# Performance work log

Measured on AMD Instinct MI355X. Metric: run time of the kernel, lower is better.

The kernel has to match this reference:

```python
import jax, jax.numpy as jnp
import numpy as np
from jax import lax

B, T, C, F_IN = 32, 2048, 64, 8
CONV_F, ATT_D, HID, N_CLS = 32, 32, 128, 4


def layer_norm(x, scale, bias, eps=1e-6):
    mu = jnp.mean(x, axis=-1, keepdims=True)
    var = jnp.mean(jnp.square(x - mu), axis=-1, keepdims=True)
    return (x - mu) * lax.rsqrt(var + eps) * scale + bias


def setup_inputs() -> dict:
    key = jax.random.key(0)
    ks = jax.random.split(key, 12)
    s = lambda *sh: 1.0 / np.sqrt(sh[-2] if len(sh) > 1 else sh[-1])
    inp = {
        "X": jax.random.normal(ks[0], (B, T, C, F_IN), jnp.float32),
        "conv_w": jax.random.normal(ks[1], (5, 1, F_IN, CONV_F), jnp.float32) * 0.1,
        "conv_b": jnp.zeros((CONV_F,), jnp.float32),
        "ln1_s": jnp.ones((CONV_F,), jnp.float32),
        "ln1_b": jnp.zeros((CONV_F,), jnp.float32),
        "q_w": jax.random.normal(ks[2], (CONV_F, ATT_D), jnp.float32) * s(CONV_F, ATT_D),
        "q_b": jnp.zeros((ATT_D,), jnp.float32),
        "k_w": jax.random.normal(ks[3], (CONV_F, ATT_D), jnp.float32) * s(CONV_F, ATT_D),
        "k_b": jnp.zeros((ATT_D,), jnp.float32),
        "ca_w": jax.random.normal(ks[4], (C, C), jnp.float32) * s(C, C),
        "ca_b": jnp.zeros((C,), jnp.float32),
        "mix_w": jax.random.normal(ks[5], (C * CONV_F, HID), jnp.float32) * s(C * CONV_F, HID),
        "mix_b": jnp.zeros((HID,), jnp.float32),
        "ln2_s": jnp.ones((HID,), jnp.float32),
        "ln2_b": jnp.zeros((HID,), jnp.float32),
        "decay_logit": jnp.full((1, HID), 2.0, jnp.float32),
        "fc_w": jax.random.normal(ks[6], (HID, HID), jnp.float32) * s(HID, HID),
        "fc_b": jnp.zeros((HID,), jnp.float32),
        "out_w": jax.random.normal(ks[7], (HID, N_CLS), jnp.float32) * s(HID, N_CLS),
        "out_b": jnp.zeros((N_CLS,), jnp.float32),
        "train": False,
    }
    return inp


def reference(X, conv_w, conv_b, ln1_s, ln1_b, q_w, q_b, k_w, k_b, ca_w, ca_b,
              mix_w, mix_b, ln2_s, ln2_b, decay_logit, fc_w, fc_b, out_w, out_b, train):
    # eval mode (train=False): no input noise, dropout is identity
    # conv: (B,T,C,F_in) -> (B,T/2,C,32), SAME padding, stride (2,1)
    Xc = lax.conv_general_dilated(X, conv_w, window_strides=(2, 1), padding='SAME',
                                  dimension_numbers=('NHWC', 'HWIO', 'NHWC')) + conv_b
    Xc = jax.nn.relu(Xc)
    Xc = layer_norm(Xc, ln1_s, ln1_b)

    # dynamic graph attention over channel axis
    x_spat = jnp.mean(Xc, axis=1)                         # (B,C,32)
    q = x_spat @ q_w + q_b
    k = x_spat @ k_w + k_b
    adj = jax.nn.softmax(jnp.einsum('bcf,bdf->bcd', q, k) / jnp.sqrt(jnp.float32(ATT_D)), axis=-1)
    Xg = jnp.einsum('bcd,btdf->btcf', adj, Xc)            # (B,T2,C,32)

    # channel gating
    ca = jax.nn.sigmoid(jnp.mean(Xc, axis=(1, 3)) @ ca_w + ca_b)  # (B,C)
    Xr = Xg * ca[:, None, :, None] + Xc

    b, t2 = Xr.shape[0], Xr.shape[1]
    Xf = Xr.reshape(b, t2, -1)                            # (B,T2,2048)
    Xm = jax.nn.relu(Xf @ mix_w + mix_b)
    Xm = layer_norm(Xm, ln2_s, ln2_b)                     # (B,T2,128)

    # LIF spiking recurrence over time
    decay = jax.nn.sigmoid(decay_logit)                   # (1,128)

    def step(mem, xt):
        mem = mem * decay + xt
        spk = (mem - 0.5 > 0).astype(mem.dtype)
        mem = mem - spk * 0.5
        return mem, spk

    _, spk_seq = lax.scan(step, jnp.zeros((b, HID), Xm.dtype), jnp.swapaxes(Xm, 0, 1))
    spk_seq = jnp.swapaxes(spk_seq, 0, 1)                 # (B,T2,128)

    feat = jnp.mean(spk_seq, axis=1)                      # (B,128)
    feat = jax.nn.relu(feat @ fc_w + fc_b)
    logits = feat @ out_w + out_b
    return logits, jnp.mean(spk_seq)
```

## Files before the change

kernel.cpp:

```cpp
#include <hip/hip_runtime.h>
#include <math.h>

#define B_    32
#define T_    2048
#define T2_   1024
#define C_    64
#define FI_   8
#define FO_   32
#define K_    2048
#define H_    128

typedef unsigned short u16;
typedef short bf16x8 __attribute__((ext_vector_type(8)));
typedef float f32x4 __attribute__((ext_vector_type(4)));

#define OFF_XSP  ((size_t)0)
#define OFF_WTH  ((size_t)67108864)
#define OFF_A    ((size_t)77594624)
#define OFF_XM   ((size_t)77725696)

__device__ __forceinline__ float bft(float x) {
  unsigned u = __float_as_uint(x);
  u = (u + 0x7fffu + ((u >> 16) & 1u)) & 0xffff0000u;
  return __uint_as_float(u);
}
__device__ __forceinline__ unsigned bfpack(float a, float b) {
  unsigned ua = __float_as_uint(a); ua = (ua + 0x7fffu + ((ua >> 16) & 1u)) >> 16;
  unsigned ub = __float_as_uint(b); ub = (ub + 0x7fffu + ((ub >> 16) & 1u)) & 0xffff0000u;
  return ua | ub;
}
__device__ __forceinline__ unsigned cvtpk(float a, float b) {
  unsigned r;
  asm("v_cvt_pk_bf16_f32 %0, %1, %2" : "=v"(r) : "v"(a), "v"(b));
  return r;
}
__device__ __forceinline__ bf16x8 packhi(const float4& x0, const float4& x1) {
  uint4 hv = make_uint4(cvtpk(x0.x, x0.y), cvtpk(x0.z, x0.w),
                        cvtpk(x1.x, x1.y), cvtpk(x1.z, x1.w));
  return *(bf16x8*)&hv;
}
__device__ __forceinline__ void pack8(const float4& x0, const float4& x1,
                                      bf16x8& h, bf16x8& l) {
  float v[8] = {x0.x, x0.y, x0.z, x0.w, x1.x, x1.y, x1.z, x1.w};
  unsigned hu[4], lu[4];
#pragma unroll
  for (int p = 0; p < 4; ++p) {
    const float a = v[2*p], b2 = v[2*p+1];
    const unsigned ph = cvtpk(a, b2);
    hu[p] = ph;
    const float fa_ = __uint_as_float(ph << 16);
    const float fb_ = __uint_as_float(ph & 0xffff0000u);
    lu[p] = cvtpk(a - fa_, b2 - fb_);
  }
  uint4 hv = make_uint4(hu[0], hu[1], hu[2], hu[3]);
  uint4 lv = make_uint4(lu[0], lu[1], lu[2], lu[3]);
  h = *(bf16x8*)&hv; l = *(bf16x8*)&lv;
}

__device__ __forceinline__ void glds16(const u16* g, u16* l) {
  auto gp = reinterpret_cast<const __attribute__((address_space(1))) unsigned int*>(
      reinterpret_cast<uintptr_t>(g));
  auto lp = reinterpret_cast<__attribute__((address_space(3))) unsigned int*>(
      reinterpret_cast<uintptr_t>(l));
  __builtin_amdgcn_global_load_lds(gp, lp, 16, 0, 0);
}

__global__ __launch_bounds__(256, 3) void k1_conv_ln(
    const float* __restrict__ X, const float* __restrict__ Wc,
    const float* __restrict__ bc, const float* __restrict__ g1,
    const float* __restrict__ be1, float* __restrict__ xsp)
{
  __shared__ float xred[4][1056];
  const int tid = threadIdx.x;
  const int w = tid >> 6, lane = tid & 63;
  const int q = lane >> 4, cl = lane & 15;
  const int chalf = w & 1, rng = w >> 1;
  const int b = blockIdx.y, tile = blockIdx.x;
  const int cbase = chalf * 32;

  bf16x8 Wh[2][2], Wl[2][2];
#pragma unroll
  for (int s = 0; s < 2; ++s)
#pragma unroll
    for (int mt = 0; mt < 2; ++mt) {
      const int f = mt * 16 + cl;
      float x8[8];
#pragma unroll
      for (int j = 0; j < 8; ++j) {
        float wv;
        if (s == 0) {
          wv = Wc[(q * 8 + j) * 32 + f];
        } else {
          wv = 0.f;
          if (q == 0) wv = Wc[(32 + j) * 32 + f];
          if (q == 1 && j == 0) wv = bc[f];
        }
        x8[j] = wv;
      }
      unsigned hu[4], lu[4];
#pragma unroll
      for (int p = 0; p < 4; ++p) {
        const float a0 = x8[2*p], a1 = x8[2*p+1];
        hu[p] = bfpack(a0, a1);
        lu[p] = bfpack(a0 - bft(a0), a1 - bft(a1));
      }
      uint4 hv = make_uint4(hu[0], hu[1], hu[2], hu[3]);
      uint4 lv = make_uint4(lu[0], lu[1], lu[2], lu[3]);
      Wh[s][mt] = *(bf16x8*)&hv;
      Wl[s][mt] = *(bf16x8*)&lv;
    }

  float g1r[2][4], be1r[2][4];
#pragma unroll
  for (int mt = 0; mt < 2; ++mt)
#pragma unroll
    for (int r = 0; r < 4; ++r) {
      const int f = mt * 16 + 4 * q + r;
      g1r[mt][r] = g1[f];
      be1r[mt][r] = be1[f];
    }

  float sacc[2][2][4];
#pragma unroll
  for (int mt = 0; mt < 2; ++mt)
#pragma unroll
    for (int nt = 0; nt < 2; ++nt)
#pragma unroll
      for (int r = 0; r < 4; ++r) sacc[mt][nt][r] = 0.f;

  const float* Xb = X + (size_t)b * T_ * C_ * FI_;
  const float4 z4f = make_float4(0.f, 0.f, 0.f, 0.f);
  const int c0g = cbase + cl, c1g = cbase + 16 + cl;

  float4 A0, A1, A2, A3, A4, A5, A6, A7;
  float4 B0, B1, B2, B3, B4, B5, B6, B7;

  auto LD = [&](int it, float4& v0, float4& v1, float4& v2, float4& v3,
                        float4& v4, float4& v5, float4& v6, float4& v7) {
    const int t2 = tile * 16 + rng * 8 + it;
    const int r0 = 2 * t2 + q - 1, r1 = 2 * t2 + 3;
    const bool ok0 = (r0 >= 0) && (r0 < T_);
    const bool ok1 = (q == 0) && (r1 < T_);
    v0 = z4f; v1 = z4f; v2 = z4f; v3 = z4f;
    v4 = z4f; v5 = z4f; v6 = z4f; v7 = z4f;
    if (ok0) {
      const float* p = Xb + (size_t)r0 * (C_ * FI_);
      v0 = *(const float4*)(p + c0g * FI_);
      v1 = *(const float4*)(p + c0g * FI_ + 4);
      v4 = *(const float4*)(p + c1g * FI_);
      v5 = *(const float4*)(p + c1g * FI_ + 4);
    }
    if (ok1) {
      const float* p = Xb + (size_t)r1 * (C_ * FI_);
      v2 = *(const float4*)(p + c0g * FI_);
      v3 = *(const float4*)(p + c0g * FI_ + 4);
      v6 = *(const float4*)(p + c1g * FI_);
      v7 = *(const float4*)(p + c1g * FI_ + 4);
    }
  };

  auto CMP = [&](const float4& v0, const float4& v1, const float4& v2,
                 const float4& v3, const float4& v4, const float4& v5,
                 const float4& v6, const float4& v7) {
    f32x4 acc[2][2];
#pragma unroll
    for (int mt = 0; mt < 2; ++mt)
#pragma unroll
      for (int nt = 0; nt < 2; ++nt) acc[mt][nt] = (f32x4){0.f,0.f,0.f,0.f};

#pragma unroll
    for (int nt = 0; nt < 2; ++nt) {
      bf16x8 Bh0 = packhi(nt ? v4 : v0, nt ? v5 : v1);
      bf16x8 Bh1 = packhi(nt ? v6 : v2, nt ? v7 : v3);
      if (q == 1) Bh1[0] = (short)0x3F80;
#pragma unroll
      for (int mt = 0; mt < 2; ++mt) {
        acc[mt][nt] = __builtin_amdgcn_mfma_f32_16x16x32_bf16(Wh[0][mt], Bh0, acc[mt][nt], 0, 0, 0);
        acc[mt][nt] = __builtin_amdgcn_mfma_f32_16x16x32_bf16(Wl[0][mt], Bh0, acc[mt][nt], 0, 0, 0);
        acc[mt][nt] = __builtin_amdgcn_mfma_f32_16x16x32_bf16(Wh[1][mt], Bh1, acc[mt][nt], 0, 0, 0);
        acc[mt][nt] = __builtin_amdgcn_mfma_f32_16x16x32_bf16(Wl[1][mt], Bh1, acc[mt][nt], 0, 0, 0);
      }
    }
#pragma unroll
    for (int nt = 0; nt < 2; ++nt) {
      float v[2][4];
      float s1 = 0.f, s2 = 0.f;
#pragma unroll
      for (int mt = 0; mt < 2; ++mt)
#pragma unroll
        for (int r = 0; r < 4; ++r) {
          const float vv = fmaxf(acc[mt][nt][r], 0.f);
          v[mt][r] = vv; s1 += vv; s2 = fmaf(vv, vv, s2);
        }
      s1 += __shfl_xor(s1, 16); s2 += __shfl_xor(s2, 16);
      s1 += __shfl_xor(s1, 32); s2 += __shfl_xor(s2, 32);
      const float mu = s1 * (1.f / 32.f);
      const float var = s2 * (1.f / 32.f) - mu * mu;
      const float rs = rsqrtf(var + 1e-6f);
#pragma unroll
      for (int mt = 0; mt < 2; ++mt)
#pragma unroll
        for (int r = 0; r < 4; ++r)
          sacc[mt][nt][r] += (v[mt][r] - mu) * rs * g1r[mt][r] + be1r[mt][r];
    }
  };

  LD(0, A0, A1, A2, A3, A4, A5, A6, A7);
#pragma unroll 1
  for (int it = 0; it < 8; it += 2) {
    if (it + 1 < 8) LD(it + 1, B0, B1, B2, B3, B4, B5, B6, B7);
    CMP(A0, A1, A2, A3, A4, A5, A6, A7);
    if (it + 2 < 8) LD(it + 2, A0, A1, A2, A3, A4, A5, A6, A7);
    CMP(B0, B1, B2, B3, B4, B5, B6, B7);
  }

#pragma unroll
  for (int mt = 0; mt < 2; ++mt)
#pragma unroll
    for (int nt = 0; nt < 2; ++nt)
#pragma unroll
      for (int r = 0; r < 4; ++r)
        xred[w][(nt * 16 + cl) * 33 + mt * 16 + 4 * q + r] = sacc[mt][nt][r];
  __syncthreads();
  if (w < 2) {
#pragma unroll
    for (int mt = 0; mt < 2; ++mt)
#pragma unroll
      for (int nt = 0; nt < 2; ++nt)
#pragma unroll
        for (int r = 0; r < 4; ++r) {
          const int idx = (nt * 16 + cl) * 33 + mt * 16 + 4 * q + r;
          const float vv = xred[w][idx] + xred[w + 2][idx];
          xsp[((size_t)b * 64 + tile) * 2048 +
              (size_t)(w * 32 + nt * 16 + cl) * 32 + mt * 16 + 4 * q + r] = vv;
        }
  }
}

__global__ __launch_bounds__(256) void k2_graph(
    const float* __restrict__ xsp, const float* __restrict__ qw,
    const float* __restrict__ qb, const float* __restrict__ kw,
    const float* __restrict__ kb, const float* __restrict__ caw,
    const float* __restrict__ cab, float* __restrict__ Aout)
{
  __shared__ float xs[64 * 32];
  __shared__ float qs[64][32];
  __shared__ float ks[64][32];
  __shared__ float sc[64][64];
  __shared__ float cain[64];
  __shared__ float cav[64];
  const int tid = threadIdx.x;
  const int b = blockIdx.x;

  for (int idx = tid; idx < 2048; idx += 256) {
    float s = 0.f;
    for (int p = 0; p < 64; ++p) s += xsp[((size_t)b * 64 + p) * 2048 + idx];
    xs[idx] = s * (1.f / (float)T2_);
  }
  __syncthreads();

  if (tid < 64) {
    float s = 0.f;
#pragma unroll
    for (int f = 0; f < 32; ++f) s += xs[tid * 32 + f];
    cain[tid] = s * (1.f / 32.f);
  }
  {
    const int cc = tid >> 2, part = tid & 3;
    float aq[8], ak[8];
#pragma unroll
    for (int j = 0; j < 8; ++j) { aq[j] = qb[part*8+j]; ak[j] = kb[part*8+j]; }
    for (int f = 0; f < 32; ++f) {
      const float xv = xs[cc * 32 + f];
#pragma unroll
      for (int j = 0; j < 8; ++j) {
        aq[j] = fmaf(xv, qw[f * 32 + part*8+j], aq[j]);
        ak[j] = fmaf(xv, kw[f * 32 + part*8+j], ak[j]);
      }
    }
#pragma unroll
    for (int j = 0; j < 8; ++j) { qs[cc][part*8+j] = aq[j]; ks[cc][part*8+j] = ak[j]; }
  }
  __syncthreads();
  {
    const int cc = tid >> 2, part = tid & 3;
    for (int dd = part * 16; dd < part * 16 + 16; ++dd) {
      float s = 0.f;
#pragma unroll
      for (int e = 0; e < 32; ++e) s = fmaf(qs[cc][e], ks[dd][e], s);
      sc[cc][dd] = s * 0.1767766953f;
    }
  }
  __syncthreads();
  if (tid < 64) {
    const int cc = tid;
    float m = -1e30f;
    for (int d = 0; d < 64; ++d) m = fmaxf(m, sc[cc][d]);
    float sum = 0.f;
    for (int d = 0; d < 64; ++d) { float e = expf(sc[cc][d] - m); sc[cc][d] = e; sum += e; }
    const float inv = 1.f / sum;
    for (int d = 0; d < 64; ++d) sc[cc][d] *= inv;
    float a = cab[cc];
    for (int d = 0; d < 64; ++d) a = fmaf(cain[d], caw[d * 64 + cc], a);
    cav[cc] = 1.f / (1.f + expf(-a));
  }
  __syncthreads();
  for (int idx = tid; idx < 4096; idx += 256) {
    const int cc = idx >> 6, dd = idx & 63;
    Aout[(size_t)b * 4096 + idx] = cav[cc] * sc[cc][dd] + (cc == dd ? 1.f : 0.f);
  }
}

__global__ __launch_bounds__(256) void k3_weff(
    const float* __restrict__ Aout, const float* __restrict__ mixw,
    u16* __restrict__ Wth)
{
  __shared__ float Ap[4096];
  __shared__ float Ms[2048];
  const int tid = threadIdx.x;
  const int b = blockIdx.x >> 5, ht = blockIdx.x & 31;
  const int d = tid & 63, hl = tid >> 6;
  const int h0 = ht * 4;
  const float* Ab = Aout + (size_t)b * 4096;
#pragma unroll
  for (int l = 0; l < 16; ++l) Ap[tid + 256 * l] = Ab[tid + 256 * l];

  float acc[32];
#pragma unroll
  for (int j = 0; j < 32; ++j) acc[j] = 0.f;

  for (int c0 = 0; c0 < 64; c0 += 16) {
    __syncthreads();
    {
      const int i0 = tid * 8;
#pragma unroll
      for (int qd = 0; qd < 2; ++qd) {
        const int i = i0 + qd * 4;
        const int cc = i >> 7, f = (i >> 2) & 31;
        const float4 v = *(const float4*)&mixw[((size_t)((c0+cc)*32 + f))*128 + h0];
        float* mp = &Ms[cc * 128 + f];
        mp[0] = v.x; mp[32] = v.y; mp[64] = v.z; mp[96] = v.w;
      }
    }
    __syncthreads();
#pragma unroll 4
    for (int cc = 0; cc < 16; ++cc) {
      const float a = Ap[(c0 + cc) * 64 + d];
      const float* mrow = &Ms[cc * 128 + hl * 32];
#pragma unroll
      for (int fq = 0; fq < 8; ++fq) {
        const f32x4 m = *(const f32x4*)&mrow[fq * 4];
        acc[fq*4+0] = fmaf(a, m[0], acc[fq*4+0]);
        acc[fq*4+1] = fmaf(a, m[1], acc[fq*4+1]);
        acc[fq*4+2] = fmaf(a, m[2], acc[fq*4+2]);
        acc[fq*4+3] = fmaf(a, m[3], acc[fq*4+3]);
      }
    }
  }

  const int h = h0 + hl;
  const size_t obase = ((size_t)(b * 64 + d) * 128 + h) * 32;
#pragma unroll
  for (int g = 0; g < 4; ++g) {
    unsigned hq[4];
#pragma unroll
    for (int jj = 0; jj < 4; ++jj)
      hq[jj] = bfpack(acc[8*g + 2*jj], acc[8*g + 2*jj + 1]);
    const int pg = (g ^ hl ^ (ht & 3)) * 8;
    *(uint4*)(Wth + obase + pg) = make_uint4(hq[0], hq[1], hq[2], hq[3]);
  }
}

__global__ __launch_bounds__(256, 2) void k4_fused(
    const float* __restrict__ X, const float* __restrict__ Wc,
    const float* __restrict__ bc, const float* __restrict__ g1,
    const float* __restrict__ be1,
    const u16* __restrict__ Bgh,
    const float* __restrict__ mixb, const float* __restrict__ g2,
    const float* __restrict__ be2, float* __restrict__ Xm)
{
  __shared__ __align__(16) u16 lds[18432];
  __shared__ float part[64 * 8];
  __shared__ float murs[128];

  const int tid = threadIdx.x;
  const int w = tid >> 6, lane = tid & 63;
  const int q = lane >> 4, cl = lane & 15;
  const int x = blockIdx.x;
  const int swz = (x & 7) * 64 + (x >> 3);
  const int b = swz >> 4, mt = swz & 15;
  const int m0 = mt * 64;

  bf16x8 Wh[2][2], Wl[2][2];
#pragma unroll
  for (int s = 0; s < 2; ++s)
#pragma unroll
    for (int m2 = 0; m2 < 2; ++m2) {
      const int f = m2 * 16 + cl;
      float x8[8];
#pragma unroll
      for (int j = 0; j < 8; ++j) {
        float wv;
        if (s == 0) {
          wv = Wc[(q * 8 + j) * 32 + f];
        } else {
          wv = 0.f;
          if (q == 0) wv = Wc[(32 + j) * 32 + f];
          if (q == 1 && j == 0) wv = bc[f];
        }
        x8[j] = wv;
      }
      unsigned hu[4], lu[4];
#pragma unroll
      for (int p = 0; p < 4; ++p) {
        const float a0 = x8[2*p], a1 = x8[2*p+1];
        hu[p] = bfpack(a0, a1);
        lu[p] = bfpack(a0 - bft(a0), a1 - bft(a1));
      }
      uint4 hv = make_uint4(hu[0], hu[1], hu[2], hu[3]);
      uint4 lv = make_uint4(lu[0], lu[1], lu[2], lu[3]);
      Wh[s][m2] = *(bf16x8*)&hv;
      Wl[s][m2] = *(bf16x8*)&lv;
    }
  float g1r[2][4], be1r[2][4];
#pragma unroll
  for (int m2 = 0; m2 < 2; ++m2)
#pragma unroll
    for (int r = 0; r < 4; ++r) {
      const int f = m2 * 16 + 4 * q + r;
      g1r[m2][r] = g1[f];
      be1r[m2][r] = be1[f];
    }

  f32x4 acc[4][2];
#pragma unroll
  for (int i = 0; i < 4; ++i)
#pragma unroll
    for (int j = 0; j < 2; ++j) acc[i][j] = (f32x4){0.f, 0.f, 0.f, 0.f};

  const int lrow = lane >> 2, lg = lane & 3;
  const size_t brow0 = (size_t)b * 262144 + (size_t)(w * 16 + lrow) * 32 + lg * 8;
  const int dA = w * 512;
  const int faA = cl * 40 + q * 8;
  const int faB = cl * 32 + ((q ^ (cl & 3) ^ (cl >> 2)) * 8);
  const float* Xb = X + (size_t)b * T_ * (C_ * FI_);
  const int t2 = m0 + w * 16 + cl;
  const int t2loc = w * 16 + cl;

  const int r0 = 2 * t2 + q - 1, r1 = 2 * t2 + 3;
  const bool ok0 = (r0 >= 0) && (r0 < T_);
  const bool ok1 = (q == 0) && (r1 < T_);
  const float* rp0 = Xb + (size_t)(ok0 ? r0 : 0) * (C_ * FI_);
  const float* rp1 = Xb + (size_t)(ok1 ? r1 : 0) * (C_ * FI_);
  const float4 z4f = make_float4(0.f, 0.f, 0.f, 0.f);

  float4 A0a, A1a, B0a, B1a;
  float4 A0b, A1b, B0b, B1b;

  auto LOADX = [&](float4& X0, float4& X1, float4& Y0, float4& Y1, int c) {
    X0 = z4f; X1 = z4f; Y0 = z4f; Y1 = z4f;
    if (ok0) { const float* p = rp0 + c * FI_; X0 = *(const float4*)p; X1 = *(const float4*)(p + 4); }
    if (ok1) { const float* p = rp1 + c * FI_; Y0 = *(const float4*)p; Y1 = *(const float4*)(p + 4); }
  };

  auto CONV = [&](const float4& X0, const float4& X1,
                  const float4& Y0, const float4& Y1, int nb) {
    bf16x8 Bh0, Bl0, Bh1, Bl1;
    pack8(X0, X1, Bh0, Bl0);
    pack8(Y0, Y1, Bh1, Bl1);
    if (q == 1) Bh1[0] = (short)0x3F80;
    f32x4 ca0 = (f32x4){0.f,0.f,0.f,0.f}, ca1 = ca0;
    ca0 = __builtin_amdgcn_mfma_f32_16x16x32_bf16(Wh[0][0], Bh0, ca0, 0, 0, 0);
    ca1 = __builtin_amdgcn_mfma_f32_16x16x32_bf16(Wh[0][1], Bh0, ca1, 0, 0, 0);
    ca0 = __builtin_amdgcn_mfma_f32_16x16x32_bf16(Wh[0][0], Bl0, ca0, 0, 0, 0);
    ca1 = __builtin_amdgcn_mfma_f32_16x16x32_bf16(Wh[0][1], Bl0, ca1, 0, 0, 0);
    ca0 = __builtin_amdgcn_mfma_f32_16x16x32_bf16(Wl[0][0], Bh0, ca0, 0, 0, 0);
    ca1 = __builtin_amdgcn_mfma_f32_16x16x32_bf16(Wl[0][1], Bh0, ca1, 0, 0, 0);
    ca0 = __builtin_amdgcn_mfma_f32_16x16x32_bf16(Wh[1][0], Bh1, ca0, 0, 0, 0);
    ca1 = __builtin_amdgcn_mfma_f32_16x16x32_bf16(Wh[1][1], Bh1, ca1, 0, 0, 0);
    ca0 = __builtin_amdgcn_mfma_f32_16x16x32_bf16(Wh[1][0], Bl1, ca0, 0, 0, 0);
    ca1 = __builtin_amdgcn_mfma_f32_16x16x32_bf16(Wh[1][1], Bl1, ca1, 0, 0, 0);
    ca0 = __builtin_amdgcn_mfma_f32_16x16x32_bf16(Wl[1][0], Bh1, ca0, 0, 0, 0);
    ca1 = __builtin_amdgcn_mfma_f32_16x16x32_bf16(Wl[1][1], Bh1, ca1, 0, 0, 0);
    float v[2][4];
    float s1 = 0.f, s2 = 0.f;
#pragma unroll
    for (int r = 0; r < 4; ++r) {
      float vv = fmaxf(ca0[r], 0.f); v[0][r] = vv; s1 += vv; s2 = fmaf(vv, vv, s2);
      vv = fmaxf(ca1[r], 0.f);       v[1][r] = vv; s1 += vv; s2 = fmaf(vv, vv, s2);
    }
    s1 += __shfl_xor(s1, 16); s2 += __shfl_xor(s2, 16);
    s1 += __shfl_xor(s1, 32); s2 += __shfl_xor(s2, 32);
    const float mu = s1 * (1.f / 32.f);
    const float var = s2 * (1.f / 32.f) - mu * mu;
    const float rs = rsqrtf(var + 1e-6f);
    const int ab = nb * 5120;
#pragma unroll
    for (int m2 = 0; m2 < 2; ++m2) {
      float y[4];
#pragma unroll
      for (int r = 0; r < 4; ++r)
        y[r] = (v[m2][r] - mu) * rs * g1r[m2][r] + be1r[m2][r];
      const unsigned h0 = cvtpk(y[0], y[1]);
      const unsigned h1 = cvtpk(y[2], y[3]);
      const float f00 = __uint_as_float(h0 << 16);
      const float f01 = __uint_as_float(h0 & 0xffff0000u);
      const float f10 = __uint_as_float(h1 << 16);
      const float f11 = __uint_as_float(h1 & 0xffff0000u);
      const unsigned l0 = cvtpk(y[0] - f00, y[1] - f01);
      const unsigned l1 = cvtpk(y[2] - f10, y[3] - f11);
      const int phys = 2 * m2 + (q >> 1);
      const int off = ab + t2loc * 40 + phys * 8 + (q & 1) * 4;
      *(uint2*)&lds[off] = make_uint2(h0, h1);
      *(uint2*)&lds[off + 2560] = make_uint2(l0, l1);
    }
  };

#define STAGE_B(kt, nb) do {                                                 \
    const int bb_ = 10240 + (nb) * 4096;                                     \
    glds16(Bgh + brow0 + (size_t)(kt) * 4096,        &lds[bb_ + dA]);        \
    glds16(Bgh + brow0 + (size_t)(kt) * 4096 + 2048, &lds[bb_ + 2048 + dA]); \
  } while (0)

  auto GEMM = [&](int nb) {
    const int ab = nb * 5120, bb = 10240 + nb * 4096;
    bf16x8 ah[4], al[4], bh[2];
#pragma unroll
    for (int mf = 0; mf < 4; ++mf) {
      ah[mf] = *(const bf16x8*)&lds[ab + mf * 640 + faA];
      al[mf] = *(const bf16x8*)&lds[ab + 2560 + mf * 640 + faA];
    }
#pragma unroll
    for (int nf = 0; nf < 2; ++nf)
      bh[nf] = *(const bf16x8*)&lds[bb + w * 1024 + nf * 512 + faB];
#pragma unroll
    for (int mf = 0; mf < 4; ++mf)
#pragma unroll
      for (int nf = 0; nf < 2; ++nf) {
        acc[mf][nf] = __builtin_amdgcn_mfma_f32_16x16x32_bf16(ah[mf], bh[nf], acc[mf][nf], 0, 0, 0);
        acc[mf][nf] = __builtin_amdgcn_mfma_f32_16x16x32_bf16(al[mf], bh[nf], acc[mf][nf], 0, 0, 0);
      }
  };

  LOADX(A0a, A1a, B0a, B1a, 0);
  STAGE_B(0, 0);
  LOADX(A0b, A1b, B0b, B1b, 1);
  CONV(A0a, A1a, B0a, B1a, 0);
  __syncthreads();

  for (int kt = 0; kt < 64; kt += 2) {
    if (kt + 2 < 64) LOADX(A0a, A1a, B0a, B1a, kt + 2);
    STAGE_B(kt + 1, 1);
    GEMM(0);
    CONV(A0b, A1b, B0b, B1b, 1);
    __syncthreads();
    if (kt + 3 < 64) LOADX(A0b, A1b, B0b, B1b, kt + 3);
    if (kt + 2 < 64) STAGE_B(kt + 2, 0);
    GEMM(1);
    if (kt + 2 < 64) CONV(A0a, A1a, B0a, B1a, 0);
    __syncthreads();
  }
#undef STAGE_B

  const int c0 = w * 32 + (lane & 15);
  const float bias0 = mixb[c0], bias1 = mixb[c0 + 16];
#pragma unroll
  for (int mf = 0; mf < 4; ++mf)
#pragma unroll
    for (int r = 0; r < 4; ++r) {
      float v0 = fmaxf(acc[mf][0][r] + bias0, 0.f);
      float v1 = fmaxf(acc[mf][1][r] + bias1, 0.f);
      acc[mf][0][r] = v0; acc[mf][1][r] = v1;
      float s1 = v0 + v1, s2 = v0 * v0 + v1 * v1;
      s1 += __shfl_xor(s1, 1);  s2 += __shfl_xor(s2, 1);
      s1 += __shfl_xor(s1, 2);  s2 += __shfl_xor(s2, 2);
      s1 += __shfl_xor(s1, 4);  s2 += __shfl_xor(s2, 4);
      s1 += __shfl_xor(s1, 8);  s2 += __shfl_xor(s2, 8);
      if ((lane & 15) == 0) {
        const int row = mf * 16 + (lane >> 4) * 4 + r;
        part[row * 8 + w * 2] = s1;
        part[row * 8 + w * 2 + 1] = s2;
      }
    }
  __syncthreads();
  if (tid < 64) {
    const float s1 = part[tid*8] + part[tid*8+2] + part[tid*8+4] + part[tid*8+6];
    const float s2 = part[tid*8+1] + part[tid*8+3] + part[tid*8+5] + part[tid*8+7];
    const float mu = s1 * (1.f / 128.f);
    const float var = s2 * (1.f / 128.f) - mu * mu;
    murs[tid * 2] = mu;
    murs[tid * 2 + 1] = rsqrtf(var + 1e-6f);
  }
  __syncthreads();
  const float g20 = g2[c0], g21 = g2[c0 + 16];
  const float b20 = be2[c0], b21 = be2[c0 + 16];
#pragma unroll
  for (int mf = 0; mf < 4; ++mf)
#pragma unroll
    for (int r = 0; r < 4; ++r) {
      const int row = mf * 16 + (lane >> 4) * 4 + r;
      const float mu = murs[row * 2], rs = murs[row * 2 + 1];
      float* op = Xm + (size_t)(b * 1024 + m0 + row) * 128;
      op[c0]      = (acc[mf][0][r] - mu) * rs * g20 + b20;
      op[c0 + 16] = (acc[mf][1][r] - mu) * rs * g21 + b21;
    }
}

__global__ __launch_bounds__(64) void k5_lif(
    const float* __restrict__ Xm, const float* __restrict__ dl,
    float* __restrict__ fs)
{
  const int id = blockIdx.x * 64 + threadIdx.x;
  const int b = id >> 7, h = id & 127;
  const float decay = 1.f / (1.f + expf(-dl[h]));
  float mem = 0.f, cnt = 0.f;
  const float* p = Xm + (size_t)b * T2_ * H_ + h;
#pragma unroll 16
  for (int t = 0; t < T2_; ++t) {
    const float xv = p[(size_t)t * H_];
    mem = fmaf(mem, decay, xv);
    const float sp = ((mem - 0.5f) > 0.f) ? 1.f : 0.f;
    cnt += sp;
    mem -= 0.5f * sp;
  }
  fs[b * H_ + h] = cnt;
}

__global__ __launch_bounds__(256) void k6_head(
    const float* __restrict__ fs, const float* __restrict__ fcw,
    const float* __restrict__ fcb, const float* __restrict__ ow,
    const float* __restrict__ ob, float* __restrict__ out)
{
  __shared__ float f[32 * 128];
  __shared__ float fr[32 * 128];
  __shared__ float red[256];
  const int tid = threadIdx.x;
  float tot = 0.f;
  for (int idx = tid; idx < 4096; idx += 256) {
    const float v = fs[idx];
    f[idx] = v * (1.f / (float)T2_);
    tot += v;
  }
  red[tid] = tot;
  __syncthreads();
  for (int s = 128; s > 0; s >>= 1) {
    if (tid < s) red[tid] += red[tid + s];
    __syncthreads();
  }
  {
    const int bb = tid >> 3, og = tid & 7;
    float a[16];
#pragma unroll
    for (int j = 0; j < 16; ++j) a[j] = fcb[og * 16 + j];
    for (int hh = 0; hh < 128; ++hh) {
      const float fv = f[bb * 128 + hh];
#pragma unroll
      for (int j = 0; j < 16; ++j)
        a[j] = fmaf(fv, fcw[hh * 128 + og * 16 + j], a[j]);
    }
#pragma unroll
    for (int j = 0; j < 16; ++j) fr[bb * 128 + og * 16 + j] = fmaxf(a[j], 0.f);
  }
  __syncthreads();
  if (tid < 128) {
    const int bb = tid >> 2, cls = tid & 3;
    float a = ob[cls];
    for (int o = 0; o < 128; ++o) a = fmaf(fr[bb * 128 + o], ow[o * 4 + cls], a);
    out[bb * 4 + cls] = a;
  }
  if (tid == 0) out[128] = red[0] * (1.f / (4096.f * 1024.f));
}

extern "C" void kernel_launch(void* const* d_in, const int* in_sizes, int n_in,
                              void* d_out, int out_size, void* d_ws, size_t ws_size,
                              hipStream_t stream) {
  const float* X     = (const float*)d_in[0];
  const float* convw = (const float*)d_in[1];
  const float* convb = (const float*)d_in[2];
  const float* ln1s  = (const float*)d_in[3];
  const float* ln1b  = (const float*)d_in[4];
  const float* qw    = (const float*)d_in[5];
  const float* qb    = (const float*)d_in[6];
  const float* kw    = (const float*)d_in[7];
  const float* kb    = (const float*)d_in[8];
  const float* caw   = (const float*)d_in[9];
  const float* cab   = (const float*)d_in[10];
  const float* mixw  = (const float*)d_in[11];
  const float* mixb  = (const float*)d_in[12];
  const float* ln2s  = (const float*)d_in[13];
  const float* ln2b  = (const float*)d_in[14];
  const float* dl    = (const float*)d_in[15];
  const float* fcw   = (const float*)d_in[16];
  const float* fcb   = (const float*)d_in[17];
  const float* outw  = (const float*)d_in[18];
  const float* outb  = (const float*)d_in[19];

  float* ws  = (float*)d_ws;
  float* xsp = ws + OFF_XSP;
  u16* Wth   = (u16*)(ws + OFF_WTH);
  float* Aou = ws + OFF_A;
  float* Xm  = ws + OFF_XM;
  float* fs  = ws + OFF_A;

  dim3 g1(64, 32);
  k1_conv_ln<<<g1, 256, 0, stream>>>(X, convw, convb, ln1s, ln1b, xsp);
  k2_graph<<<32, 256, 0, stream>>>(xsp, qw, qb, kw, kb, caw, cab, Aou);
  k3_weff<<<1024, 256, 0, stream>>>(Aou, mixw, Wth);
  k4_fused<<<512, 256, 0, stream>>>(X, convw, convb, ln1s, ln1b,
                                    Wth, mixb, ln2s, ln2b, Xm);
  k5_lif<<<64, 64, 0, stream>>>(Xm, dl, fs);
  k6_head<<<1, 256, 0, stream>>>(fs, fcw, fcb, outw, outb, (float*)d_out);
}
```

Baseline: 292.9 us.

## Split k4 K-loop across two wave groups with LDS reduction

Doubles the k4_fused block to 512 threads. Two groups of four waves each take half of the 64 K-steps, using separate LDS buffers. The partial accumulators are then summed through LDS before the bias, ReLU, LayerNorm and store epilogue. The aim is more waves per tile to hide latency in the conv+GEMM pipeline. The cost is a doubled LDS footprint, an extra exchange and barrier, and half the threads idle in the epilogue.

```diff
diff --git a/kernel.cpp b/kernel.cpp
--- a/kernel.cpp
+++ b/kernel.cpp
@@ -371,7 +371,7 @@
   }
 }
 
-__global__ __launch_bounds__(256, 2) void k4_fused(
+__global__ __launch_bounds__(512) void k4_fused(
     const float* __restrict__ X, const float* __restrict__ Wc,
     const float* __restrict__ bc, const float* __restrict__ g1,
     const float* __restrict__ be1,
@@ -379,17 +379,20 @@
     const float* __restrict__ mixb, const float* __restrict__ g2,
     const float* __restrict__ be2, float* __restrict__ Xm)
 {
-  __shared__ __align__(16) u16 lds[18432];
+  __shared__ __align__(16) u16 lds[36864];
   __shared__ float part[64 * 8];
   __shared__ float murs[128];
 
   const int tid = threadIdx.x;
   const int w = tid >> 6, lane = tid & 63;
+  const int wv = w & 3, g = w >> 2;
   const int q = lane >> 4, cl = lane & 15;
   const int x = blockIdx.x;
   const int swz = (x & 7) * 64 + (x >> 3);
   const int b = swz >> 4, mt = swz & 15;
   const int m0 = mt * 64;
+  const int ks0 = g * 32;
+  const int GB = g * 18432;
 
   bf16x8 Wh[2][2], Wl[2][2];
 #pragma unroll
@@ -400,15 +403,15 @@
       float x8[8];
 #pragma unroll
       for (int j = 0; j < 8; ++j) {
-        float wv;
+        float wvx;
         if (s == 0) {
-          wv = Wc[(q * 8 + j) * 32 + f];
+          wvx = Wc[(q * 8 + j) * 32 + f];
         } else {
-          wv = 0.f;
-          if (q == 0) wv = Wc[(32 + j) * 32 + f];
-          if (q == 1 && j == 0) wv = bc[f];
+          wvx = 0.f;
+          if (q == 0) wvx = Wc[(32 + j) * 32 + f];
+          if (q == 1 && j == 0) wvx = bc[f];
         }
-        x8[j] = wv;
+        x8[j] = wvx;
       }
       unsigned hu[4], lu[4];
 #pragma unroll
@@ -439,13 +442,13 @@
     for (int j = 0; j < 2; ++j) acc[i][j] = (f32x4){0.f, 0.f, 0.f, 0.f};
 
   const int lrow = lane >> 2, lg = lane & 3;
-  const size_t brow0 = (size_t)b * 262144 + (size_t)(w * 16 + lrow) * 32 + lg * 8;
-  const int dA = w * 512;
+  const size_t brow0 = (size_t)b * 262144 + (size_t)(wv * 16 + lrow) * 32 + lg * 8;
+  const int dA = wv * 512;
   const int faA = cl * 40 + q * 8;
   const int faB = cl * 32 + ((q ^ (cl & 3) ^ (cl >> 2)) * 8);
   const float* Xb = X + (size_t)b * T_ * (C_ * FI_);
-  const int t2 = m0 + w * 16 + cl;
-  const int t2loc = w * 16 + cl;
+  const int t2 = m0 + wv * 16 + cl;
+  const int t2loc = wv * 16 + cl;
 
   const int r0 = 2 * t2 + q - 1, r1 = 2 * t2 + 3;
   const bool ok0 = (r0 >= 0) && (r0 < T_);
@@ -494,7 +497,7 @@
     const float mu = s1 * (1.f / 32.f);
     const float var = s2 * (1.f / 32.f) - mu * mu;
     const float rs = rsqrtf(var + 1e-6f);
-    const int ab = nb * 5120;
+    const int ab = GB + nb * 5120;
 #pragma unroll
     for (int m2 = 0; m2 < 2; ++m2) {
       float y[4];
@@ -516,14 +519,14 @@
     }
   };
 
-#define STAGE_B(kt, nb) do {                                                 \
-    const int bb_ = 10240 + (nb) * 4096;                                     \
-    glds16(Bgh + brow0 + (size_t)(kt) * 4096,        &lds[bb_ + dA]);        \
-    glds16(Bgh + brow0 + (size_t)(kt) * 4096 + 2048, &lds[bb_ + 2048 + dA]); \
+#define STAGE_B(ktg, nb) do {                                                \
+    const int bb_ = GB + 10240 + (nb) * 4096;                                \
+    glds16(Bgh + brow0 + (size_t)(ktg) * 4096,        &lds[bb_ + dA]);       \
+    glds16(Bgh + brow0 + (size_t)(ktg) * 4096 + 2048, &lds[bb_ + 2048 + dA]);\
   } while (0)
 
   auto GEMM = [&](int nb) {
-    const int ab = nb * 5120, bb = 10240 + nb * 4096;
+    const int ab = GB + nb * 5120, bb = GB + 10240 + nb * 4096;
     bf16x8 ah[4], al[4], bh[2];
 #pragma unroll
     for (int mf = 0; mf < 4; ++mf) {
@@ -532,7 +535,7 @@
     }
 #pragma unroll
     for (int nf = 0; nf < 2; ++nf)
-      bh[nf] = *(const bf16x8*)&lds[bb + w * 1024 + nf * 512 + faB];
+      bh[nf] = *(const bf16x8*)&lds[bb + wv * 1024 + nf * 512 + faB];
 #pragma unroll
     for (int mf = 0; mf < 4; ++mf)
 #pragma unroll
@@ -542,46 +545,70 @@
       }
   };
 
-  LOADX(A0a, A1a, B0a, B1a, 0);
-  STAGE_B(0, 0);
-  LOADX(A0b, A1b, B0b, B1b, 1);
+  LOADX(A0a, A1a, B0a, B1a, ks0 + 0);
+  STAGE_B(ks0 + 0, 0);
+  LOADX(A0b, A1b, B0b, B1b, ks0 + 1);
   CONV(A0a, A1a, B0a, B1a, 0);
   __syncthreads();
 
-  for (int kt = 0; kt < 64; kt += 2) {
-    if (kt + 2 < 64) LOADX(A0a, A1a, B0a, B1a, kt + 2);
-    STAGE_B(kt + 1, 1);
+  for (int kt = 0; kt < 32; kt += 2) {
+    if (kt + 2 < 32) LOADX(A0a, A1a, B0a, B1a, ks0 + kt + 2);
+    STAGE_B(ks0 + kt + 1, 1);
     GEMM(0);
     CONV(A0b, A1b, B0b, B1b, 1);
     __syncthreads();
-    if (kt + 3 < 64) LOADX(A0b, A1b, B0b, B1b, kt + 3);
-    if (kt + 2 < 64) STAGE_B(kt + 2, 0);
+    if (kt + 3 < 32) LOADX(A0b, A1b, B0b, B1b, ks0 + kt + 3);
+    if (kt + 2 < 32) STAGE_B(ks0 + kt + 2, 0);
     GEMM(1);
-    if (kt + 2 < 64) CONV(A0a, A1a, B0a, B1a, 0);
+    if (kt + 2 < 32) CONV(A0a, A1a, B0a, B1a, 0);
     __syncthreads();
   }
 #undef STAGE_B
 
-  const int c0 = w * 32 + (lane & 15);
+  float* exch = (float*)lds;
+  if (g == 1) {
+    const int l8 = tid & 255;
+#pragma unroll
+    for (int mf = 0; mf < 4; ++mf)
+#pragma unroll
+      for (int nf = 0; nf < 2; ++nf)
+#pragma unroll
+        for (int r = 0; r < 4; ++r)
+          exch[l8 * 33 + mf * 8 + nf * 4 + r] = acc[mf][nf][r];
+  }
+  __syncthreads();
+  if (g == 0) {
+#pragma unroll
+    for (int mf = 0; mf < 4; ++mf)
+#pragma unroll
+      for (int nf = 0; nf < 2; ++nf)
+#pragma unroll
+        for (int r = 0; r < 4; ++r)
+          acc[mf][nf][r] += exch[tid * 33 + mf * 8 + nf * 4 + r];
+  }
+
+  const int c0 = wv * 32 + (lane & 15);
   const float bias0 = mixb[c0], bias1 = mixb[c0 + 16];
-#pragma unroll
-  for (int mf = 0; mf < 4; ++mf)
-#pragma unroll
-    for (int r = 0; r < 4; ++r) {
-      float v0 = fmaxf(acc[mf][0][r] + bias0, 0.f);
-      float v1 = fmaxf(acc[mf][1][r] + bias1, 0.f);
-      acc[mf][0][r] = v0; acc[mf][1][r] = v1;
-      float s1 = v0 + v1, s2 = v0 * v0 + v1 * v1;
-      s1 += __shfl_xor(s1, 1);  s2 += __shfl_xor(s2, 1);
-      s1 += __shfl_xor(s1, 2);  s2 += __shfl_xor(s2, 2);
-      s1 += __shfl_xor(s1, 4);  s2 += __shfl_xor(s2, 4);
-      s1 += __shfl_xor(s1, 8);  s2 += __shfl_xor(s2, 8);
-      if ((lane & 15) == 0) {
-        const int row = mf * 16 + (lane >> 4) * 4 + r;
-        part[row * 8 + w * 2] = s1;
-        part[row * 8 + w * 2 + 1] = s2;
-      }
-    }
+  if (g == 0) {
+#pragma unroll
+    for (int mf = 0; mf < 4; ++mf)
+#pragma unroll
+      for (int r = 0; r < 4; ++r) {
+        float v0 = fmaxf(acc[mf][0][r] + bias0, 0.f);
+        float v1 = fmaxf(acc[mf][1][r] + bias1, 0.f);
+        acc[mf][0][r] = v0; acc[mf][1][r] = v1;
+        float s1 = v0 + v1, s2 = v0 * v0 + v1 * v1;
+        s1 += __shfl_xor(s1, 1);  s2 += __shfl_xor(s2, 1);
+        s1 += __shfl_xor(s1, 2);  s2 += __shfl_xor(s2, 2);
+        s1 += __shfl_xor(s1, 4);  s2 += __shfl_xor(s2, 4);
+        s1 += __shfl_xor(s1, 8);  s2 += __shfl_xor(s2, 8);
+        if ((lane & 15) == 0) {
+          const int row = mf * 16 + (lane >> 4) * 4 + r;
+          part[row * 8 + wv * 2] = s1;
+          part[row * 8 + wv * 2 + 1] = s2;
+        }
+      }
+  }
   __syncthreads();
   if (tid < 64) {
     const float s1 = part[tid*8] + part[tid*8+2] + part[tid*8+4] + part[tid*8+6];
@@ -592,18 +619,20 @@
     murs[tid * 2 + 1] = rsqrtf(var + 1e-6f);
   }
   __syncthreads();
-  const float g20 = g2[c0], g21 = g2[c0 + 16];
-  const float b20 = be2[c0], b21 = be2[c0 + 16];
-#pragma unroll
-  for (int mf = 0; mf < 4; ++mf)
-#pragma unroll
-    for (int r = 0; r < 4; ++r) {
-      const int row = mf * 16 + (lane >> 4) * 4 + r;
-      const float mu = murs[row * 2], rs = murs[row * 2 + 1];
-      float* op = Xm + (size_t)(b * 1024 + m0 + row) * 128;
-      op[c0]      = (acc[mf][0][r] - mu) * rs * g20 + b20;
-      op[c0 + 16] = (acc[mf][1][r] - mu) * rs * g21 + b21;
-    }
+  if (g == 0) {
+    const float g20 = g2[c0], g21 = g2[c0 + 16];
+    const float b20 = be2[c0], b21 = be2[c0 + 16];
+#pragma unroll
+    for (int mf = 0; mf < 4; ++mf)
+#pragma unroll
+      for (int r = 0; r < 4; ++r) {
+        const int row = mf * 16 + (lane >> 4) * 4 + r;
+        const float mu = murs[row * 2], rs = murs[row * 2 + 1];
+        float* op = Xm + (size_t)(b * 1024 + m0 + row) * 128;
+        op[c0]      = (acc[mf][0][r] - mu) * rs * g20 + b20;
+        op[c0 + 16] = (acc[mf][1][r] - mu) * rs * g21 + b21;
+      }
+  }
 }
 
 __global__ __launch_bounds__(64) void k5_lif(
@@ -706,7 +735,7 @@
   k1_conv_ln<<<g1, 256, 0, stream>>>(X, convw, convb, ln1s, ln1b, xsp);
   k2_graph<<<32, 256, 0, stream>>>(xsp, qw, qb, kw, kb, caw, cab, Aou);
   k3_weff<<<1024, 256, 0, stream>>>(Aou, mixw, Wth);
-  k4_fused<<<512, 256, 0, stream>>>(X, convw, convb, ln1s, ln1b,
+  k4_fused<<<512, 512, 0, stream>>>(X, convw, convb, ln1s, ln1b,
                                     Wth, mixb, ln2s, ln2b, Xm);
   k5_lif<<<64, 64, 0, stream>>>(Xm, dl, fs);
   k6_head<<<1, 256, 0, stream>>>(fs, fcw, fcb, outw, outb, (float*)d_out);
```

Result: slower. 312.7 us (+6.8%).
